# Optimization experiments

Measured on AMD Instinct MI355X. Metric: run time of the kernel, lower is better.

The kernel has to match this reference:

```python
import jax, jax.numpy as jnp
import numpy as np

# Model config (mirrors init_kwargs)
E = 8          # num_experts
K = 2          # top_k
S = 1          # select_top_k
THRESHOLD = 0.7
NORM_TOPK = True
H = 1024       # hidden_dim
F = 1024       # moe intermediate dim
B, SEQ = 2, 1024


def setup_inputs() -> dict:
    key = jax.random.key(0)
    k1, k2, k3, k4, k5 = jax.random.split(key, 5)
    hidden_states = jax.random.normal(k1, (B, SEQ, H), jnp.float32)
    gate_weight = jax.random.normal(k2, (E, H), jnp.float32) * 0.02
    gate_up_proj = jax.random.normal(k3, (E, 2 * F, H), jnp.float32) * 0.02
    down_proj = jax.random.normal(k4, (E, H, F), jnp.float32) * 0.02
    sim = jax.random.uniform(k5, (E, E), jnp.float32)
    sim = (sim + sim.T) / 2.0
    sim = sim.at[jnp.arange(E), jnp.arange(E)].set(1.0)  # fill_diagonal_(1.0)
    return {
        "hidden_states": hidden_states,
        "gate_weight": gate_weight,
        "gate_up_proj": gate_up_proj,
        "down_proj": down_proj,
        "similarity_matrix": sim,
    }


def reference(hidden_states, gate_weight, gate_up_proj, down_proj, similarity_matrix):
    b, s, h = hidden_states.shape
    x = hidden_states.reshape(-1, h)                     # [N, H]
    N = x.shape[0]

    # Router: logits -> softmax(fp32) -> topk (+ optional norm)
    logits = x @ gate_weight.T                           # [N, E]
    probs = jax.nn.softmax(logits.astype(jnp.float32), axis=-1)
    top_w, top_i = jax.lax.top_k(probs, K)               # [N, K]
    if NORM_TOPK:
        top_w = top_w / jnp.clip(jnp.sum(top_w, -1, keepdims=True), 1e-12)

    # SERE reroute: primary = union of top-S experts over batch; map each
    # secondary expert to its most-similar primary if sim >= threshold.
    primary_mask = jnp.zeros((E,), bool).at[top_i[:, :S].reshape(-1)].set(True)
    sim = jnp.where(primary_mask[None, :], similarity_matrix.astype(jnp.float32), -jnp.inf)
    best_j = jnp.argmax(sim, axis=-1)                    # best primary per expert
    best_sim = jnp.max(sim, axis=-1)
    ids = jnp.arange(E)
    expert_map = jnp.where((~primary_mask) & (best_sim >= THRESHOLD), best_j, ids)
    rerouted = expert_map[top_i]                         # [N, K]

    # Merge duplicate slots via scatter-add, then re-topk K.
    rows = jnp.arange(N)[:, None]
    dense = jnp.zeros((N, E), top_w.dtype).at[rows, rerouted].add(top_w)
    fw, fi = jax.lax.top_k(dense, K)                     # nnz per row <= K, so topk keeps all
    combine = jnp.zeros((N, E), fw.dtype).at[rows, fi].add(jnp.where(fw > 0, fw, 0.0))  # [N, E]

    # Expert MLPs (dense jit-friendly dispatch): silu(gate)*up -> down
    gu = jnp.einsum('nh,efh->enf', x, gate_up_proj)      # [E, N, 2F]
    g, u = jnp.split(gu, 2, axis=-1)
    hmid = jax.nn.silu(g) * u                            # [E, N, F]
    y = jnp.einsum('enf,ehf->enh', hmid, down_proj)      # [E, N, H]
    out = jnp.einsum('ne,enh->nh', combine, y)           # weighted combine
    return out.reshape(b, s, h)
```

## Files before the change

kernel.cpp:

```cpp
#include <hip/hip_runtime.h>
#include <cstdint>
#include <cstddef>

#define N_TOK 2048
#define HID 1024
#define FDIM 1024
#define NE 8
#define PAIR_CAP 5120
#define MT 128
#define BK 64
#define THRESH 0.7f

typedef __attribute__((ext_vector_type(8))) short bf16x8;
typedef __attribute__((ext_vector_type(4))) float f32x4;

static __device__ __forceinline__ unsigned short f2bf(float f) {
  unsigned int u = __float_as_uint(f);
  u += 0x7FFF + ((u >> 16) & 1);
  return (unsigned short)(u >> 16);
}
static __device__ __forceinline__ float bf2f(unsigned short u) {
  return __uint_as_float(((unsigned int)u) << 16);
}

static __device__ __forceinline__ void gl2lds16(const unsigned short* g, unsigned short* l) {
  __builtin_amdgcn_global_load_lds(
      (const __attribute__((address_space(1))) void*)g,
      (__attribute__((address_space(3))) void*)l, 16, 0, 0);
}

__global__ __launch_bounds__(256) void k_cvt(
    const float* __restrict__ src, unsigned short* __restrict__ dst, int n4) {
  int i = blockIdx.x * 256 + threadIdx.x;
  if (i < n4) {
    float4 v = ((const float4*)src)[i];
    ushort4 o;
    o.x = f2bf(v.x); o.y = f2bf(v.y); o.z = f2bf(v.z); o.w = f2bf(v.w);
    ((ushort4*)dst)[i] = o;
  }
}

__global__ __launch_bounds__(256) void k_router(
    const float* __restrict__ x, const float* __restrict__ gw,
    unsigned short* __restrict__ xb, float* __restrict__ topw,
    int* __restrict__ topi) {
  __shared__ float sgw[NE * HID];
  int t = threadIdx.x;
#pragma unroll
  for (int i = 0; i < NE * HID / 256; ++i) sgw[t + 256 * i] = gw[t + 256 * i];
  __syncthreads();
  int lane = t & 63;
  int wave = t >> 6;
  int n = blockIdx.x * 4 + wave;
  float acc[NE];
#pragma unroll
  for (int e = 0; e < NE; ++e) acc[e] = 0.f;
#pragma unroll
  for (int i = 0; i < HID / 64; ++i) {
    int h = i * 64 + lane;
    float xv = x[(size_t)n * HID + h];
    xb[(size_t)n * HID + h] = f2bf(xv);
#pragma unroll
    for (int e = 0; e < NE; ++e) acc[e] += xv * sgw[e * HID + h];
  }
#pragma unroll
  for (int off = 32; off > 0; off >>= 1) {
#pragma unroll
    for (int e = 0; e < NE; ++e) acc[e] += __shfl_xor(acc[e], off, 64);
  }
  if (lane == 0) {
    float m = acc[0];
    for (int e = 1; e < NE; ++e) m = fmaxf(m, acc[e]);
    float p[NE]; float s = 0.f;
    for (int e = 0; e < NE; ++e) { p[e] = __expf(acc[e] - m); s += p[e]; }
    float inv = 1.f / s;
    for (int e = 0; e < NE; ++e) p[e] *= inv;
    int i0 = 0; float b0 = p[0];
    for (int e = 1; e < NE; ++e) if (p[e] > b0) { b0 = p[e]; i0 = e; }
    int i1 = -1; float b1 = -1.f;
    for (int e = 0; e < NE; ++e) { if (e == i0) continue; if (p[e] > b1) { b1 = p[e]; i1 = e; } }
    float sw = b0 + b1; if (sw < 1e-12f) sw = 1e-12f;
    topw[n * 2] = b0 / sw; topw[n * 2 + 1] = b1 / sw;
    topi[n * 2] = i0;      topi[n * 2 + 1] = i1;
  }
}

__global__ __launch_bounds__(256) void k_pairs(
    const float* __restrict__ sim, const int* __restrict__ topi,
    const float* __restrict__ topw, int* __restrict__ ctrl,
    int* __restrict__ ptok, float* __restrict__ pw, int* __restrict__ pot) {
  __shared__ int prim[NE], emap[NE], cnt[NE], soff[NE], cur[NE], padc[NE];
  int t = threadIdx.x;
  if (t < NE) { prim[t] = 0; cnt[t] = 0; }
  __syncthreads();
  for (int n = t; n < N_TOK; n += 256) prim[topi[n * 2]] = 1;
  __syncthreads();
  if (t < NE) {
    float best = -1e30f; int bj = -1;
    for (int j = 0; j < NE; ++j) {
      if (prim[j]) {
        float s = sim[t * NE + j];
        if (s > best) { best = s; bj = j; }
      }
    }
    int m = t;
    if (!prim[t] && bj >= 0 && best >= THRESH) m = bj;
    emap[t] = m;
  }
  __syncthreads();
  for (int n = t; n < N_TOK; n += 256) {
    atomicAdd(&cnt[emap[topi[n * 2]]], 1);
    atomicAdd(&cnt[emap[topi[n * 2 + 1]]], 1);
  }
  __syncthreads();
  if (t == 0) {
    int o = 0;
    for (int e = 0; e < NE; ++e) {
      soff[e] = o;
      int p = (cnt[e] + MT - 1) & ~(MT - 1);
      padc[e] = p; cur[e] = 0; o += p;
    }
    ctrl[1] = o >> 7;
  }
  __syncthreads();
  if (t < NE) { ctrl[24 + t] = soff[t]; ctrl[32 + t] = padc[t]; }
  if (t < 40) {
    int slot = t << 7;
    int e = 0;
    for (int j = 0; j < NE; ++j)
      if (slot >= soff[j] && slot < soff[j] + padc[j]) e = j;
    ctrl[64 + t] = e;
  }
  for (int n = t; n < N_TOK; n += 256) {
    int i0 = topi[n * 2], i1 = topi[n * 2 + 1];
    int e0 = emap[i0], e1 = emap[i1];
    int s0 = soff[e0] + atomicAdd(&cur[e0], 1);
    int s1 = soff[e1] + atomicAdd(&cur[e1], 1);
    ptok[s0] = n; pw[s0] = topw[n * 2];
    ptok[s1] = n; pw[s1] = topw[n * 2 + 1];
    pot[n * 2] = s0; pot[n * 2 + 1] = s1;
  }
  __syncthreads();
  for (int e = 0; e < NE; ++e) {
    for (int s = cnt[e] + t; s < padc[e]; s += 256) {
      ptok[soff[e] + s] = 0; pw[soff[e] + s] = 0.f;
    }
  }
}


__global__ __launch_bounds__(256, 2) void k_gemm1(
    const unsigned short* __restrict__ xb, const unsigned short* __restrict__ gupb,
    unsigned short* __restrict__ hmid, const int* __restrict__ ptok,
    const int* __restrict__ ctrl) {
  int b = blockIdx.x;
  int tl = b >> 5;
  int y = b & 31;
  if (tl >= ctrl[1]) return;
  int e = ctrl[64 + tl];
  int base = tl * MT;
  int f0 = y * 32;

  __shared__ unsigned short As[2][MT * BK];
  __shared__ unsigned short Bs[2][64 * BK];
  __shared__ int toks[MT];

  int t = threadIdx.x;
  if (t < MT) toks[t] = ptok[base + t];
  __syncthreads();

  int lane = t & 63;
  int wave = t >> 6;
  int wm = wave >> 1, wn = wave & 1;
  int lm = lane & 15, lh = lane >> 4;

  f32x4 acc[4][2] = {};
  const unsigned short* gbase = gupb + (size_t)e * 2 * FDIM * HID;

  auto stage = [&](int k0, int bi) {
#pragma unroll
    for (int i = 0; i < 4; ++i) {
      int q = i * 256 + t;
      int r = q >> 3;
      int cl = (q & 7) ^ (r & 7);
      gl2lds16(xb + (size_t)toks[r] * HID + k0 + cl * 8, &As[bi][(q & ~63) * 8]);
    }
#pragma unroll
    for (int i = 0; i < 2; ++i) {
      int q = i * 256 + t;
      int r = q >> 3;
      int cl = (q & 7) ^ (r & 7);
      int grow = ((r >> 4) & 1) * FDIM + f0 + ((r >> 5) << 4) + (r & 15);
      gl2lds16(gbase + (size_t)grow * HID + k0 + cl * 8, &Bs[bi][(q & ~63) * 8]);
    }
  };

  stage(0, 0);
  stage(BK, 1);

  for (int k = 0; k < 16; ++k) {
    if (k < 15) asm volatile("s_waitcnt vmcnt(6)" ::: "memory");
    else        asm volatile("s_waitcnt vmcnt(0)" ::: "memory");
    asm volatile("s_barrier" ::: "memory");
    int bi = k & 1;
#pragma unroll
    for (int kk = 0; kk < 2; ++kk) {
      bf16x8 af[4], bfr[2];
#pragma unroll
      for (int rb = 0; rb < 4; ++rb) {
        int row = wm * 64 + rb * 16 + lm;
        int p = (kk * 4 + lh) ^ (row & 7);
        af[rb] = *(const bf16x8*)(&As[bi][row * BK + p * 8]);
      }
#pragma unroll
      for (int cc = 0; cc < 2; ++cc) {
        int row = wn * 32 + cc * 16 + lm;
        int p = (kk * 4 + lh) ^ (row & 7);
        bfr[cc] = *(const bf16x8*)(&Bs[bi][row * BK + p * 8]);
      }
#pragma unroll
      for (int rb = 0; rb < 4; ++rb) {
#pragma unroll
        for (int cc = 0; cc < 2; ++cc)
          acc[rb][cc] = __builtin_amdgcn_mfma_f32_16x16x32_bf16(af[rb], bfr[cc], acc[rb][cc], 0, 0, 0);
      }
    }
    if (k < 14) {
      asm volatile("s_waitcnt lgkmcnt(0)" ::: "memory");
      asm volatile("s_barrier" ::: "memory");
      stage((k + 2) * BK, bi);
    }
  }
#pragma unroll
  for (int rb = 0; rb < 4; ++rb) {
    int slot = base + wm * 64 + rb * 16 + lh * 4;
    f32x4 g = acc[rb][0];
    f32x4 u = acc[rb][1];
    int f = f0 + wn * 16 + lm;
#pragma unroll
    for (int reg = 0; reg < 4; ++reg) {
      float gv = g[reg];
      float hm = gv / (1.f + __expf(-gv)) * u[reg];
      hmid[(size_t)(slot + reg) * FDIM + f] = f2bf(hm);
    }
  }
}

__global__ __launch_bounds__(256, 2) void k_gemm2(
    const unsigned short* __restrict__ hmid, const unsigned short* __restrict__ dwnb,
    unsigned short* __restrict__ yb, const int* __restrict__ ctrl) {
  int b = blockIdx.x;
  int tl = b >> 5;
  int y = b & 31;
  if (tl >= ctrl[1]) return;
  int e = ctrl[64 + tl];
  int base = tl * MT;
  int h0 = y * 32;

  __shared__ unsigned short As[2][MT * BK];
  __shared__ unsigned short Bs[2][32 * BK];

  int t = threadIdx.x;
  int lane = t & 63;
  int wave = t >> 6;
  int wm = wave >> 1, wn = wave & 1;
  int lm = lane & 15, lh = lane >> 4;

  f32x4 acc[4] = {};
  const unsigned short* dbase = dwnb + (size_t)e * HID * FDIM;

  auto stage = [&](int k0, int bi) {
#pragma unroll
    for (int i = 0; i < 4; ++i) {
      int q = i * 256 + t;
      int r = q >> 3;
      int cl = (q & 7) ^ (r & 7);
      gl2lds16(hmid + (size_t)(base + r) * FDIM + k0 + cl * 8, &As[bi][(q & ~63) * 8]);
    }
    {
      int q = t;
      int r = q >> 3;
      int cl = (q & 7) ^ (r & 7);
      gl2lds16(dbase + (size_t)(h0 + r) * FDIM + k0 + cl * 8, &Bs[bi][(q & ~63) * 8]);
    }
  };

  stage(0, 0);
  stage(BK, 1);

  for (int k = 0; k < 16; ++k) {
    if (k < 15) asm volatile("s_waitcnt vmcnt(5)" ::: "memory");
    else        asm volatile("s_waitcnt vmcnt(0)" ::: "memory");
    asm volatile("s_barrier" ::: "memory");
    int bi = k & 1;
#pragma unroll
    for (int kk = 0; kk < 2; ++kk) {
      bf16x8 af[4], bfr;
#pragma unroll
      for (int rb = 0; rb < 4; ++rb) {
        int row = wm * 64 + rb * 16 + lm;
        int p = (kk * 4 + lh) ^ (row & 7);
        af[rb] = *(const bf16x8*)(&As[bi][row * BK + p * 8]);
      }
      {
        int row = wn * 16 + lm;
        int p = (kk * 4 + lh) ^ (row & 7);
        bfr = *(const bf16x8*)(&Bs[bi][row * BK + p * 8]);
      }
#pragma unroll
      for (int rb = 0; rb < 4; ++rb)
        acc[rb] = __builtin_amdgcn_mfma_f32_16x16x32_bf16(af[rb], bfr, acc[rb], 0, 0, 0);
    }
    if (k < 14) {
      asm volatile("s_waitcnt lgkmcnt(0)" ::: "memory");
      asm volatile("s_barrier" ::: "memory");
      stage((k + 2) * BK, bi);
    }
  }
#pragma unroll
  for (int rb = 0; rb < 4; ++rb) {
    int slot = base + wm * 64 + rb * 16 + lh * 4;
    int h = h0 + wn * 16 + lm;
#pragma unroll
    for (int reg = 0; reg < 4; ++reg)
      yb[(size_t)(slot + reg) * HID + h] = f2bf(acc[rb][reg]);
  }
}

__global__ __launch_bounds__(256) void k_combine(
    const unsigned short* __restrict__ yb, const float* __restrict__ pw,
    const int* __restrict__ pot, float* __restrict__ out) {
  int n = blockIdx.x;
  int t = threadIdx.x;
  int p0 = pot[n * 2], p1 = pot[n * 2 + 1];
  float w0 = pw[p0], w1 = pw[p1];
  int h = t * 4;
  ushort4 a = *(const ushort4*)(yb + (size_t)p0 * HID + h);
  ushort4 b = *(const ushort4*)(yb + (size_t)p1 * HID + h);
  float4 o;
  o.x = w0 * bf2f(a.x) + w1 * bf2f(b.x);
  o.y = w0 * bf2f(a.y) + w1 * bf2f(b.y);
  o.z = w0 * bf2f(a.z) + w1 * bf2f(b.z);
  o.w = w0 * bf2f(a.w) + w1 * bf2f(b.w);
  *(float4*)(out + (size_t)n * HID + h) = o;
}

extern "C" void kernel_launch(void* const* d_in, const int* in_sizes, int n_in,
                              void* d_out, int out_size, void* d_ws, size_t ws_size,
                              hipStream_t stream) {
  (void)in_sizes; (void)n_in; (void)out_size; (void)ws_size;
  const float* x   = (const float*)d_in[0];
  const float* gw  = (const float*)d_in[1];
  const float* gup = (const float*)d_in[2];
  const float* dwn = (const float*)d_in[3];
  const float* sim = (const float*)d_in[4];
  float* out = (float*)d_out;

  char* w = (char*)d_ws;
  int* ctrl = (int*)w;
  size_t off = 512;
  unsigned short* xb = (unsigned short*)(w + off); off += (size_t)N_TOK * HID * 2;
  float* topw = (float*)(w + off); off += (size_t)N_TOK * 2 * 4;
  int*   topi = (int*)(w + off);   off += (size_t)N_TOK * 2 * 4;
  int*   ptok = (int*)(w + off);   off += (size_t)PAIR_CAP * 4;
  float* pw   = (float*)(w + off); off += (size_t)PAIR_CAP * 4;
  int*   pot  = (int*)(w + off);   off += (size_t)N_TOK * 2 * 4;
  unsigned short* hmid = (unsigned short*)(w + off); off += (size_t)PAIR_CAP * FDIM * 2;
  unsigned short* yb   = (unsigned short*)(w + off); off += (size_t)PAIR_CAP * HID * 2;
  unsigned short* gupb = (unsigned short*)(w + off); off += (size_t)NE * 2 * FDIM * HID * 2;
  unsigned short* dwnb = (unsigned short*)(w + off); off += (size_t)NE * HID * FDIM * 2;

  int n4g = NE * 2 * FDIM * HID / 4;
  int n4d = NE * HID * FDIM / 4;
  k_cvt<<<(n4g + 255) / 256, 256, 0, stream>>>(gup, gupb, n4g);
  k_cvt<<<(n4d + 255) / 256, 256, 0, stream>>>(dwn, dwnb, n4d);
  k_router<<<N_TOK / 4, 256, 0, stream>>>(x, gw, xb, topw, topi);
  k_pairs<<<1, 256, 0, stream>>>(sim, topi, topw, ctrl, ptok, pw, pot);
  k_gemm1<<<dim3(40 * 32), 256, 0, stream>>>(xb, gupb, hmid, ptok, ctrl);
  k_gemm2<<<dim3(40 * 32), 256, 0, stream>>>(hmid, dwnb, yb, ctrl);
  k_combine<<<N_TOK, 256, 0, stream>>>(yb, pw, pot, out);
}
```

Measured before the change: 214.1 us.

## Fuse fp32-to-bf16 weight conversion into expert GEMM B-tile loads

Removes the two standalone conversion kernels that turned the fp32 gate_up and down weights into bf16 copies. The GEMMs now read fp32 weights into registers, convert and pack them to bf16, and write them into swizzled LDS, with a reworked waitcnt/barrier pipeline. This avoids writing and re-reading about 48MB of bf16 weights each call. In exchange, fp32 weight tiles are re-read by every token tile (doubling B bytes per GEMM), register pressure rises, and each k-step gains extra conversion work and a barrier.

```diff
diff --git a/kernel.cpp b/kernel.cpp
--- a/kernel.cpp
+++ b/kernel.cpp
@@ -27,17 +27,6 @@
   __builtin_amdgcn_global_load_lds(
       (const __attribute__((address_space(1))) void*)g,
       (__attribute__((address_space(3))) void*)l, 16, 0, 0);
-}
-
-__global__ __launch_bounds__(256) void k_cvt(
-    const float* __restrict__ src, unsigned short* __restrict__ dst, int n4) {
-  int i = blockIdx.x * 256 + threadIdx.x;
-  if (i < n4) {
-    float4 v = ((const float4*)src)[i];
-    ushort4 o;
-    o.x = f2bf(v.x); o.y = f2bf(v.y); o.z = f2bf(v.z); o.w = f2bf(v.w);
-    ((ushort4*)dst)[i] = o;
-  }
 }
 
 __global__ __launch_bounds__(256) void k_router(
@@ -150,7 +139,7 @@
 
 
 __global__ __launch_bounds__(256, 2) void k_gemm1(
-    const unsigned short* __restrict__ xb, const unsigned short* __restrict__ gupb,
+    const unsigned short* __restrict__ xb, const float* __restrict__ gup,
     unsigned short* __restrict__ hmid, const int* __restrict__ ptok,
     const int* __restrict__ ctrl) {
   int b = blockIdx.x;
@@ -175,33 +164,45 @@
   int lm = lane & 15, lh = lane >> 4;
 
   f32x4 acc[4][2] = {};
-  const unsigned short* gbase = gupb + (size_t)e * 2 * FDIM * HID;
-
-  auto stage = [&](int k0, int bi) {
+  const float* gbase = gup + (size_t)e * 2 * FDIM * HID;
+
+  auto stageA = [&](int k0, int bi) {
 #pragma unroll
     for (int i = 0; i < 4; ++i) {
-      int q = i * 256 + t;
-      int r = q >> 3;
-      int cl = (q & 7) ^ (r & 7);
+      int q = i * 256 + t; int r = q >> 3; int cl = (q & 7) ^ (r & 7);
       gl2lds16(xb + (size_t)toks[r] * HID + k0 + cl * 8, &As[bi][(q & ~63) * 8]);
     }
-#pragma unroll
-    for (int i = 0; i < 2; ++i) {
-      int q = i * 256 + t;
-      int r = q >> 3;
-      int cl = (q & 7) ^ (r & 7);
+  };
+  float4 vb[2][4];
+  auto loadB = [&](int k0, int s) {
+#pragma unroll
+    for (int i = 0; i < 4; ++i) {
+      int q = i * 256 + t; int r = q >> 4; int c4 = q & 15;
       int grow = ((r >> 4) & 1) * FDIM + f0 + ((r >> 5) << 4) + (r & 15);
-      gl2lds16(gbase + (size_t)grow * HID + k0 + cl * 8, &Bs[bi][(q & ~63) * 8]);
-    }
-  };
-
-  stage(0, 0);
-  stage(BK, 1);
+      vb[s][i] = *(const float4*)(gbase + (size_t)grow * HID + k0 + c4 * 4);
+    }
+  };
+  auto writeB = [&](int s, int bi) {
+#pragma unroll
+    for (int i = 0; i < 4; ++i) {
+      int q = i * 256 + t; int r = q >> 4; int c4 = q & 15;
+      int pch = (c4 >> 1) ^ (r & 7);
+      unsigned long long pk = (unsigned long long)f2bf(vb[s][i].x)
+          | ((unsigned long long)f2bf(vb[s][i].y) << 16)
+          | ((unsigned long long)f2bf(vb[s][i].z) << 32)
+          | ((unsigned long long)f2bf(vb[s][i].w) << 48);
+      *(unsigned long long*)(&Bs[bi][r * BK + pch * 8 + (c4 & 1) * 4]) = pk;
+    }
+  };
+
+  loadB(0, 0); stageA(0, 0); loadB(BK, 1); stageA(BK, 1);
+  asm volatile("s_waitcnt vmcnt(12)" ::: "memory");
+  writeB(0, 0);
+  asm volatile("s_waitcnt lgkmcnt(0)" ::: "memory");
+  asm volatile("s_waitcnt vmcnt(8)" ::: "memory");
+  asm volatile("s_barrier" ::: "memory");
 
   for (int k = 0; k < 16; ++k) {
-    if (k < 15) asm volatile("s_waitcnt vmcnt(6)" ::: "memory");
-    else        asm volatile("s_waitcnt vmcnt(0)" ::: "memory");
-    asm volatile("s_barrier" ::: "memory");
     int bi = k & 1;
 #pragma unroll
     for (int kk = 0; kk < 2; ++kk) {
@@ -225,10 +226,19 @@
           acc[rb][cc] = __builtin_amdgcn_mfma_f32_16x16x32_bf16(af[rb], bfr[cc], acc[rb][cc], 0, 0, 0);
       }
     }
-    if (k < 14) {
+    if (k < 15) {
+      asm volatile("s_waitcnt vmcnt(4)" ::: "memory");
+      writeB((k + 1) & 1, bi ^ 1);
+      if (k < 14) loadB((k + 2) * BK, k & 1);
       asm volatile("s_waitcnt lgkmcnt(0)" ::: "memory");
       asm volatile("s_barrier" ::: "memory");
-      stage((k + 2) * BK, bi);
+      if (k < 14) {
+        stageA((k + 2) * BK, bi);
+        asm volatile("s_waitcnt vmcnt(8)" ::: "memory");
+      } else {
+        asm volatile("s_waitcnt vmcnt(0)" ::: "memory");
+      }
+      asm volatile("s_barrier" ::: "memory");
     }
   }
 #pragma unroll
@@ -247,7 +257,7 @@
 }
 
 __global__ __launch_bounds__(256, 2) void k_gemm2(
-    const unsigned short* __restrict__ hmid, const unsigned short* __restrict__ dwnb,
+    const unsigned short* __restrict__ hmid, const float* __restrict__ dwn,
     unsigned short* __restrict__ yb, const int* __restrict__ ctrl) {
   int b = blockIdx.x;
   int tl = b >> 5;
@@ -267,31 +277,44 @@
   int lm = lane & 15, lh = lane >> 4;
 
   f32x4 acc[4] = {};
-  const unsigned short* dbase = dwnb + (size_t)e * HID * FDIM;
-
-  auto stage = [&](int k0, int bi) {
+  const float* dbase = dwn + (size_t)e * HID * FDIM;
+
+  auto stageA = [&](int k0, int bi) {
 #pragma unroll
     for (int i = 0; i < 4; ++i) {
-      int q = i * 256 + t;
-      int r = q >> 3;
-      int cl = (q & 7) ^ (r & 7);
+      int q = i * 256 + t; int r = q >> 3; int cl = (q & 7) ^ (r & 7);
       gl2lds16(hmid + (size_t)(base + r) * FDIM + k0 + cl * 8, &As[bi][(q & ~63) * 8]);
     }
-    {
-      int q = t;
-      int r = q >> 3;
-      int cl = (q & 7) ^ (r & 7);
-      gl2lds16(dbase + (size_t)(h0 + r) * FDIM + k0 + cl * 8, &Bs[bi][(q & ~63) * 8]);
-    }
-  };
-
-  stage(0, 0);
-  stage(BK, 1);
+  };
+  float4 vb[2][2];
+  auto loadB = [&](int k0, int s) {
+#pragma unroll
+    for (int i = 0; i < 2; ++i) {
+      int q = i * 256 + t; int r = q >> 4; int c4 = q & 15;
+      vb[s][i] = *(const float4*)(dbase + (size_t)(h0 + r) * FDIM + k0 + c4 * 4);
+    }
+  };
+  auto writeB = [&](int s, int bi) {
+#pragma unroll
+    for (int i = 0; i < 2; ++i) {
+      int q = i * 256 + t; int r = q >> 4; int c4 = q & 15;
+      int pch = (c4 >> 1) ^ (r & 7);
+      unsigned long long pk = (unsigned long long)f2bf(vb[s][i].x)
+          | ((unsigned long long)f2bf(vb[s][i].y) << 16)
+          | ((unsigned long long)f2bf(vb[s][i].z) << 32)
+          | ((unsigned long long)f2bf(vb[s][i].w) << 48);
+      *(unsigned long long*)(&Bs[bi][r * BK + pch * 8 + (c4 & 1) * 4]) = pk;
+    }
+  };
+
+  loadB(0, 0); stageA(0, 0); loadB(BK, 1); stageA(BK, 1);
+  asm volatile("s_waitcnt vmcnt(10)" ::: "memory");
+  writeB(0, 0);
+  asm volatile("s_waitcnt lgkmcnt(0)" ::: "memory");
+  asm volatile("s_waitcnt vmcnt(6)" ::: "memory");
+  asm volatile("s_barrier" ::: "memory");
 
   for (int k = 0; k < 16; ++k) {
-    if (k < 15) asm volatile("s_waitcnt vmcnt(5)" ::: "memory");
-    else        asm volatile("s_waitcnt vmcnt(0)" ::: "memory");
-    asm volatile("s_barrier" ::: "memory");
     int bi = k & 1;
 #pragma unroll
     for (int kk = 0; kk < 2; ++kk) {
@@ -311,10 +334,19 @@
       for (int rb = 0; rb < 4; ++rb)
         acc[rb] = __builtin_amdgcn_mfma_f32_16x16x32_bf16(af[rb], bfr, acc[rb], 0, 0, 0);
     }
-    if (k < 14) {
+    if (k < 15) {
+      asm volatile("s_waitcnt vmcnt(4)" ::: "memory");
+      writeB((k + 1) & 1, bi ^ 1);
+      if (k < 14) loadB((k + 2) * BK, k & 1);
       asm volatile("s_waitcnt lgkmcnt(0)" ::: "memory");
       asm volatile("s_barrier" ::: "memory");
-      stage((k + 2) * BK, bi);
+      if (k < 14) {
+        stageA((k + 2) * BK, bi);
+        asm volatile("s_waitcnt vmcnt(6)" ::: "memory");
+      } else {
+        asm volatile("s_waitcnt vmcnt(0)" ::: "memory");
+      }
+      asm volatile("s_barrier" ::: "memory");
     }
   }
 #pragma unroll
@@ -367,16 +399,10 @@
   int*   pot  = (int*)(w + off);   off += (size_t)N_TOK * 2 * 4;
   unsigned short* hmid = (unsigned short*)(w + off); off += (size_t)PAIR_CAP * FDIM * 2;
   unsigned short* yb   = (unsigned short*)(w + off); off += (size_t)PAIR_CAP * HID * 2;
-  unsigned short* gupb = (unsigned short*)(w + off); off += (size_t)NE * 2 * FDIM * HID * 2;
-  unsigned short* dwnb = (unsigned short*)(w + off); off += (size_t)NE * HID * FDIM * 2;
-
-  int n4g = NE * 2 * FDIM * HID / 4;
-  int n4d = NE * HID * FDIM / 4;
-  k_cvt<<<(n4g + 255) / 256, 256, 0, stream>>>(gup, gupb, n4g);
-  k_cvt<<<(n4d + 255) / 256, 256, 0, stream>>>(dwn, dwnb, n4d);
+
   k_router<<<N_TOK / 4, 256, 0, stream>>>(x, gw, xb, topw, topi);
   k_pairs<<<1, 256, 0, stream>>>(sim, topi, topw, ctrl, ptok, pw, pot);
-  k_gemm1<<<dim3(40 * 32), 256, 0, stream>>>(xb, gupb, hmid, ptok, ctrl);
-  k_gemm2<<<dim3(40 * 32), 256, 0, stream>>>(hmid, dwnb, yb, ctrl);
+  k_gemm1<<<dim3(40 * 32), 256, 0, stream>>>(xb, gup, hmid, ptok, ctrl);
+  k_gemm2<<<dim3(40 * 32), 256, 0, stream>>>(hmid, dwn, yb, ctrl);
   k_combine<<<N_TOK, 256, 0, stream>>>(yb, pw, pot, out);
 }
```

Result: slower. 311.1 us (+45.3%).
